# Kernel optimization log

Measured on AMD Instinct MI355X. Metric: run time of the kernel, lower is better.

The kernel has to match this reference:

```python
import jax, jax.numpy as jnp
import numpy as np

NUM_CLASSES = 80
CONF_THRE = 0.2
NMS_THRE = 0.45
MAX_DET = 300   # fixed cap replacing torch's variable-length NMS output (padded + keep mask)
IMG = 640.0


def setup_inputs() -> dict:
    key = jax.random.key(0)
    k1, k2 = jax.random.split(key)
    pred = jax.random.uniform(k1, (32, 8400, 85), dtype=jnp.float32)
    # scale cx,cy,w,h to pixel range so IoU/NMS geometry is realistic
    pred = pred.at[..., :4].multiply(IMG)
    zone = jax.random.uniform(k2, (8, 2), dtype=jnp.float32) * IMG
    return {"prediction": pred, "zone": zone}


def _pairwise_iou(b):
    # b: [B, K, 4] in x1y1x2y2
    area = jnp.clip(b[..., 2] - b[..., 0], 0.0) * jnp.clip(b[..., 3] - b[..., 1], 0.0)
    lt = jnp.maximum(b[:, :, None, :2], b[:, None, :, :2])
    rb = jnp.minimum(b[:, :, None, 2:], b[:, None, :, 2:])
    wh = jnp.clip(rb - lt, 0.0)
    inter = wh[..., 0] * wh[..., 1]
    return inter / (area[:, :, None] + area[:, None, :] - inter + 1e-9)


def _postprocess(prediction):
    # decode cx,cy,w,h -> x1,y1,x2,y2
    xy = prediction[..., :2]
    wh = prediction[..., 2:4]
    boxes = jnp.concatenate([xy - wh * 0.5, xy + wh * 0.5], axis=-1)  # [B,N,4]
    obj = prediction[..., 4]                                           # [B,N]
    cls = prediction[..., 5:5 + NUM_CLASSES]
    class_conf = jnp.max(cls, axis=-1)                                 # [B,N]
    class_pred = jnp.argmax(cls, axis=-1)                              # [B,N]

    # confidence mask (obj * class_conf >= thre); invalid -> -inf so top_k drops them
    nms_score = obj * class_conf
    nms_score = jnp.where(nms_score >= CONF_THRE, nms_score, -jnp.inf)

    s, idx = jax.lax.top_k(nms_score, MAX_DET)                         # [B,K]
    b = jnp.take_along_axis(boxes, idx[..., None], axis=1)             # [B,K,4]

    # class-agnostic greedy NMS on score-sorted boxes (matches torchvision.ops.nms)
    iou = _pairwise_iou(b)                                             # [B,K,K]
    keep = jnp.isfinite(s)                                             # valid (passed conf) entries
    ar = jnp.arange(MAX_DET)
    def body(i, keep):
        sup = keep[:, i][:, None] & (iou[:, i, :] > NMS_THRE) & (ar > i)
        return keep & jnp.logical_not(sup)
    keep = jax.lax.fori_loop(0, MAX_DET, body, keep)

    obj_s = jnp.take_along_axis(obj, idx, axis=1)
    conf_s = jnp.take_along_axis(class_conf, idx, axis=1)
    cls_s = jnp.take_along_axis(class_pred, idx, axis=1).astype(jnp.int32)
    # extract_boxes_scores_and_classes: score = max over columns [obj, class_conf]
    scores = jnp.maximum(obj_s, conf_s)
    return b, scores, cls_s, keep


def _points_inside_zone(px, py, zone):
    # px, py: [B,K]; zone: [Z,2]. Ray-casting parity test (faithful to torch version).
    zr = jnp.roll(zone, shift=1, axis=0)
    xi, yi = zone[:, 0], zone[:, 1]
    xj, yj = zr[:, 0], zr[:, 1]
    pyb = py[..., None]  # [B,K,1] vs [Z]
    pxb = px[..., None]
    gyi = yi > pyb
    gyj = yj > pyb
    gx = (xj - xi) * (pyb - yi) / (yj - yi) + xi
    inter = (gyi != gyj) & (gx > pxb)
    return (jnp.sum(inter.astype(jnp.int32), axis=-1) % 2) > 0


def reference(prediction, zone):
    b, scores, classes, keep = _postprocess(prediction)
    cx = (b[..., 0] + b[..., 2]) * 0.5
    cy = (b[..., 1] + b[..., 3]) * 0.5
    in_zone = _points_inside_zone(cx, cy, zone) & keep
    centers_yx = jnp.stack([cy, cx], axis=-1)                          # [B,K,2]
    boxes_yxyx = jnp.stack([b[..., 1], b[..., 0], b[..., 3], b[..., 2]], axis=-1)
    return boxes_yxyx, in_zone, scores, classes, centers_yx, keep
```

## Files before the change

kernel.cpp:

```cpp
#include <hip/hip_runtime.h>
#include <stdint.h>

typedef unsigned long long ull;

#define NA 8400
#define NB 32
#define KTOP 300
#define NC 80
#define CH 9
#define NCOPY 16
#define HSTRIDE 257

#define O1 38400
#define O2 48000
#define O3 57600
#define O4 67200
#define O5 86400

__global__ __launch_bounds__(256) void score_kernel(const float* __restrict__ pred,
                                                    uint32_t* __restrict__ keys) {
    __shared__ float sP[128 * 85];
    const int blk = blockIdx.x;
    const float4* g4 = (const float4*)(pred + (size_t)blk * 128 * 85);
    float4* l4 = (float4*)sP;
    for (int i = threadIdx.x; i < (128 * 85 / 4); i += 256) l4[i] = g4[i];
    __syncthreads();
    const int t = threadIdx.x;
    if (t < 128) {
        const float* p = sP + t * 85;
        float obj = p[4];
        float b0 = p[5], b1 = p[6], b2 = p[7], b3 = p[8];
        #pragma unroll
        for (int c = 4; c < NC; c += 4) {
            b0 = fmaxf(b0, p[5 + c]);
            b1 = fmaxf(b1, p[6 + c]);
            b2 = fmaxf(b2, p[7 + c]);
            b3 = fmaxf(b3, p[8 + c]);
        }
        float best = fmaxf(fmaxf(b0, b1), fmaxf(b2, b3));
        float sc = obj * best;
        uint32_t u = (sc >= 0.2f) ? (__float_as_uint(sc) | 0x80000000u) : 0x007FFFFFu;
        keys[(size_t)blk * 128 + t] = u;
    }
}

__global__ __launch_bounds__(1024) void batch_kernel(const float* __restrict__ pred,
                                                     const float* __restrict__ zone,
                                                     const uint32_t* __restrict__ keys,
                                                     float* __restrict__ out) {
    #pragma clang fp contract(off)
    __shared__ union {
        uint32_t keys[8448];
        struct {
            float b0[KTOP], b1[KTOP], b2[KTOP], b3[KTOP];
            ull mask[KTOP * 5];
        } late;
    } u;
    __shared__ ull sSel[KTOP];
    __shared__ ull sSorted[KTOP];
    __shared__ uint32_t sH[NCOPY * HSTRIDE];
    __shared__ uint32_t sWTot[16];
    __shared__ uint32_t sTot4[4];
    __shared__ uint32_t sBc[2];
    __shared__ int sCnt;
    __shared__ ull sKeepF[5];
    __shared__ float sZone[16];

    const int b = blockIdx.x;
    const int t = threadIdx.x;
    const int lane = t & 63;
    const int wv = t >> 6;

    {
        const uint4* g4 = (const uint4*)(keys + (size_t)b * NA);
        uint4* l4 = (uint4*)u.keys;
        for (int i = t; i < NA / 4; i += 1024) l4[i] = g4[i];
    }
    if (t < 16) sZone[t] = zone[t];
    if (t == 0) sCnt = 0;
    __syncthreads();

    uint32_t prefix = 0, r = KTOP;
    const int beg = t * CH;
    const int end = (beg + CH < NA) ? beg + CH : NA;
    for (int round = 0; round < 4; ++round) {
        const int shift = 24 - 8 * round;
        for (int i = t; i < NCOPY * HSTRIDE; i += 1024) sH[i] = 0u;
        __syncthreads();
        const uint32_t pmask = (round == 0) ? 0u : (0xFFFFFFFFu << (shift + 8));
        for (int e = beg; e < end; ++e) {
            uint32_t k = u.keys[e];
            if ((k & pmask) == (prefix & pmask))
                atomicAdd(&sH[wv * HSTRIDE + ((k >> shift) & 0xFFu)], 1u);
        }
        __syncthreads();
        uint32_t v = 0, s = 0;
        if (t < 256) {
            #pragma unroll
            for (int c = 0; c < NCOPY; ++c) v += sH[c * HSTRIDE + t];
            s = v;
            #pragma unroll
            for (int off = 1; off < 64; off <<= 1) {
                uint32_t o = __shfl_down(s, off, 64);
                if (lane + off < 64) s += o;
            }
            if (lane == 0) sTot4[t >> 6] = s;
        }
        __syncthreads();
        if (t < 256) {
            uint32_t S = s;
            const int w4 = t >> 6;
            #pragma unroll
            for (int w2 = 0; w2 < 4; ++w2) if (w2 > w4) S += sTot4[w2];
            uint32_t above = S - v;
            if (above < r && S >= r) {
                sBc[0] = prefix | ((uint32_t)t << shift);
                sBc[1] = r - above;
            }
        }
        __syncthreads();
        prefix = sBc[0]; r = sBc[1];
    }
    const uint32_t kth = prefix;
    const uint32_t rem = r;
    const uint32_t cntgt = KTOP - rem;

    {
        uint32_t eqc = 0;
        for (int e = beg; e < end; ++e) {
            uint32_t k = u.keys[e];
            if (k > kth) {
                int p = atomicAdd(&sCnt, 1);
                sSel[p] = ((ull)k << 32) | (ull)(0xFFFFFFFFu - (uint32_t)e);
            } else if (k == kth) eqc++;
        }
        uint32_t ps = eqc;
        #pragma unroll
        for (int off = 1; off < 64; off <<= 1) {
            uint32_t o = __shfl_up(ps, off, 64);
            if (lane >= off) ps += o;
        }
        if (lane == 63) sWTot[wv] = ps;
        __syncthreads();
        uint32_t off0 = ps - eqc;
        #pragma unroll
        for (int w2 = 0; w2 < 16; ++w2) if (w2 < wv) off0 += sWTot[w2];
        for (int e = beg; e < end; ++e) {
            uint32_t k = u.keys[e];
            if (k == kth) {
                if (off0 < rem)
                    sSel[cntgt + off0] = ((ull)k << 32) | (ull)(0xFFFFFFFFu - (uint32_t)e);
                off0++;
            }
        }
        __syncthreads();
    }

    if (t < KTOP) {
        ull my = sSel[t];
        int rk = 0;
        for (int j = 0; j < KTOP; ++j) {
            ull v = sSel[j];
            rk += (v > my) ? 1 : 0;
        }
        sSorted[rk] = my;
    }
    __syncthreads();

    const size_t bo = (size_t)b * KTOP;
    if (t < KTOP) {
        uint32_t a = 0xFFFFFFFFu - (uint32_t)sSorted[t];
        const float* p = pred + ((size_t)b * NA + a) * 85;
        float x = p[0], y = p[1], w = p[2], h = p[3], obj = p[4];
        float best = p[5]; int bc = 0;
        for (int c = 1; c < NC; ++c) {
            float v = p[5 + c];
            if (v > best) { best = v; bc = c; }
        }
        float hw = w * 0.5f, hh = h * 0.5f;
        float x1 = x - hw, y1 = y - hh, x2 = x + hw, y2 = y + hh;
        u.late.b0[t] = x1; u.late.b1[t] = y1;
        u.late.b2[t] = x2; u.late.b3[t] = y2;
        out[(bo + t) * 4 + 0] = y1;
        out[(bo + t) * 4 + 1] = x1;
        out[(bo + t) * 4 + 2] = y2;
        out[(bo + t) * 4 + 3] = x2;
        out[O4 + (bo + t) * 2 + 0] = (y1 + y2) * 0.5f;
        out[O4 + (bo + t) * 2 + 1] = (x1 + x2) * 0.5f;
        out[O2 + bo + t] = fmaxf(obj, best);
        out[O3 + bo + t] = (float)bc;
    }
    __syncthreads();

    for (int p = t; p < KTOP * 5; p += 1024) {
        const int i = p / 5;
        const int role = p % 5;
        const int j0 = role * 64;
        int jmax = j0 + 64; if (jmax > KTOP) jmax = KTOP;
        float x1 = u.late.b0[i], y1 = u.late.b1[i], x2 = u.late.b2[i], y2 = u.late.b3[i];
        float ai = fmaxf(x2 - x1, 0.0f) * fmaxf(y2 - y1, 0.0f);
        ull bits = 0ull;
        int jbeg = (j0 > i + 1) ? j0 : (i + 1);
        for (int j = jbeg; j < jmax; ++j) {
            float bx1 = u.late.b0[j], by1 = u.late.b1[j], bx2 = u.late.b2[j], by2 = u.late.b3[j];
            float aj = fmaxf(bx2 - bx1, 0.0f) * fmaxf(by2 - by1, 0.0f);
            float iw = fminf(x2, bx2) - fmaxf(x1, bx1); iw = fmaxf(iw, 0.0f);
            float ih = fminf(y2, by2) - fmaxf(y1, by1); ih = fmaxf(ih, 0.0f);
            float inter = iw * ih;
            float den = ai + aj;
            den = den - inter;
            den = den + 1e-9f;
            float iou = inter / den;
            if (iou > 0.45f) bits |= (1ull << (j - j0));
        }
        u.late.mask[p] = bits;
    }
    __syncthreads();

    if (wv == 0) {
        ull rm[5][5];
        ull kw[5];
        #pragma unroll
        for (int w = 0; w < 5; ++w) {
            int i = w * 64 + lane;
            bool f = (i < KTOP) && (((uint32_t)(sSorted[i] >> 32)) > 0x007FFFFFu);
            kw[w] = __ballot(f);
            #pragma unroll
            for (int ww = 0; ww < 5; ++ww)
                rm[w][ww] = (i < KTOP) ? u.late.mask[i * 5 + ww] : 0ull;
        }
        #pragma unroll
        for (int w = 0; w < 5; ++w) {
            ull cur = kw[w];
            while (cur) {
                int ib = __builtin_ctzll(cur);
                ull m0 = __shfl(rm[w][0], ib);
                ull m1 = __shfl(rm[w][1], ib);
                ull m2 = __shfl(rm[w][2], ib);
                ull m3 = __shfl(rm[w][3], ib);
                ull m4 = __shfl(rm[w][4], ib);
                kw[0] &= ~m0; kw[1] &= ~m1; kw[2] &= ~m2; kw[3] &= ~m3; kw[4] &= ~m4;
                ull done = (ib == 63) ? 0ull : (~0ull << (ib + 1));
                cur = kw[w] & done;
            }
        }
        if (lane == 0) {
            #pragma unroll
            for (int w = 0; w < 5; ++w) sKeepF[w] = kw[w];
        }
    }
    __syncthreads();

    if (t < KTOP) {
        int kp = (int)((sKeepF[t >> 6] >> (t & 63)) & 1ull);
        float cy = (u.late.b1[t] + u.late.b3[t]) * 0.5f;
        float cx = (u.late.b0[t] + u.late.b2[t]) * 0.5f;
        int cnt = 0;
        #pragma unroll
        for (int e = 0; e < 8; ++e) {
            float xi = sZone[2 * e], yi = sZone[2 * e + 1];
            int ep = (e + 7) & 7;
            float xj = sZone[2 * ep], yj = sZone[2 * ep + 1];
            bool gyi = yi > cy, gyj = yj > cy;
            if (gyi != gyj) {
                float gx = (xj - xi) * (cy - yi) / (yj - yi) + xi;
                if (gx > cx) cnt++;
            }
        }
        int inz = (((cnt & 1) != 0) && kp) ? 1 : 0;
        out[O1 + bo + t] = (float)inz;
        out[O5 + bo + t] = (float)kp;
    }
}

extern "C" void kernel_launch(void* const* d_in, const int* in_sizes, int n_in,
                              void* d_out, int out_size, void* d_ws, size_t ws_size,
                              hipStream_t stream) {
    const float* pred = (const float*)d_in[0];
    const float* zone = (const float*)d_in[1];
    float* out = (float*)d_out;
    uint32_t* keys = (uint32_t*)d_ws;

    score_kernel<<<(NB * NA) / 128, 256, 0, stream>>>(pred, keys);
    batch_kernel<<<NB, 1024, 0, stream>>>(pred, zone, keys, out);
}
```

Measured before the change: 200.3 us.

## Keep keys in registers and parallelize selection, ranking, argmax and zone test

Each thread now holds its 9 keys in registers instead of staging all keys in shared memory. The radix histogram scan runs in a single wave with one fewer barrier. Above-threshold selection uses a packed prefix scan instead of a shared atomic counter. Rank sorting is split across four threads per element, the class argmax is split between two lanes, and the zone test overlaps with the serial NMS wave. This adds register pressure, and the IoU loop now runs over full rows with a predicate instead of starting after the diagonal.

```diff
diff --git a/kernel.cpp b/kernel.cpp
--- a/kernel.cpp
+++ b/kernel.cpp
@@ -49,20 +49,15 @@
                                                      const uint32_t* __restrict__ keys,
                                                      float* __restrict__ out) {
     #pragma clang fp contract(off)
-    __shared__ union {
-        uint32_t keys[8448];
-        struct {
-            float b0[KTOP], b1[KTOP], b2[KTOP], b3[KTOP];
-            ull mask[KTOP * 5];
-        } late;
-    } u;
+    __shared__ float sB0[KTOP], sB1[KTOP], sB2[KTOP], sB3[KTOP];
+    __shared__ ull sMask[KTOP * 5];
     __shared__ ull sSel[KTOP];
     __shared__ ull sSorted[KTOP];
     __shared__ uint32_t sH[NCOPY * HSTRIDE];
     __shared__ uint32_t sWTot[16];
-    __shared__ uint32_t sTot4[4];
     __shared__ uint32_t sBc[2];
-    __shared__ int sCnt;
+    __shared__ uint32_t sRank[KTOP];
+    __shared__ uint32_t sPar[KTOP];
     __shared__ ull sKeepF[5];
     __shared__ float sZone[16];
 
@@ -71,52 +66,54 @@
     const int lane = t & 63;
     const int wv = t >> 6;
 
-    {
-        const uint4* g4 = (const uint4*)(keys + (size_t)b * NA);
-        uint4* l4 = (uint4*)u.keys;
-        for (int i = t; i < NA / 4; i += 1024) l4[i] = g4[i];
+    uint32_t myk[CH];
+    const int beg = t * CH;
+    #pragma unroll
+    for (int e = 0; e < CH; ++e) {
+        int idx = beg + e;
+        myk[e] = (idx < NA) ? keys[(size_t)b * NA + idx] : 0u;
     }
     if (t < 16) sZone[t] = zone[t];
-    if (t == 0) sCnt = 0;
-    __syncthreads();
+    if (t < KTOP) sRank[t] = 0u;
 
     uint32_t prefix = 0, r = KTOP;
-    const int beg = t * CH;
-    const int end = (beg + CH < NA) ? beg + CH : NA;
     for (int round = 0; round < 4; ++round) {
         const int shift = 24 - 8 * round;
         for (int i = t; i < NCOPY * HSTRIDE; i += 1024) sH[i] = 0u;
         __syncthreads();
         const uint32_t pmask = (round == 0) ? 0u : (0xFFFFFFFFu << (shift + 8));
-        for (int e = beg; e < end; ++e) {
-            uint32_t k = u.keys[e];
-            if ((k & pmask) == (prefix & pmask))
+        const uint32_t pref = prefix & pmask;
+        #pragma unroll
+        for (int e = 0; e < CH; ++e) {
+            uint32_t k = myk[e];
+            if ((k & pmask) == pref)
                 atomicAdd(&sH[wv * HSTRIDE + ((k >> shift) & 0xFFu)], 1u);
         }
         __syncthreads();
-        uint32_t v = 0, s = 0;
-        if (t < 256) {
+        if (wv == 0) {
+            uint32_t v0 = 0, v1 = 0, v2 = 0, v3 = 0;
             #pragma unroll
-            for (int c = 0; c < NCOPY; ++c) v += sH[c * HSTRIDE + t];
-            s = v;
+            for (int c = 0; c < NCOPY; ++c) {
+                const uint32_t* hc = &sH[c * HSTRIDE];
+                v0 += hc[lane]; v1 += hc[64 + lane];
+                v2 += hc[128 + lane]; v3 += hc[192 + lane];
+            }
+            uint32_t s0 = v0, s1 = v1, s2 = v2, s3 = v3;
             #pragma unroll
             for (int off = 1; off < 64; off <<= 1) {
-                uint32_t o = __shfl_down(s, off, 64);
-                if (lane + off < 64) s += o;
-            }
-            if (lane == 0) sTot4[t >> 6] = s;
-        }
-        __syncthreads();
-        if (t < 256) {
-            uint32_t S = s;
-            const int w4 = t >> 6;
-            #pragma unroll
-            for (int w2 = 0; w2 < 4; ++w2) if (w2 > w4) S += sTot4[w2];
-            uint32_t above = S - v;
-            if (above < r && S >= r) {
-                sBc[0] = prefix | ((uint32_t)t << shift);
-                sBc[1] = r - above;
-            }
+                uint32_t o0 = __shfl_down(s0, off, 64), o1 = __shfl_down(s1, off, 64);
+                uint32_t o2 = __shfl_down(s2, off, 64), o3 = __shfl_down(s3, off, 64);
+                if (lane + off < 64) { s0 += o0; s1 += o1; s2 += o2; s3 += o3; }
+            }
+            uint32_t T1 = __shfl(s1, 0, 64), T2 = __shfl(s2, 0, 64), T3 = __shfl(s3, 0, 64);
+            uint32_t S0 = s0 + T1 + T2 + T3;
+            uint32_t S1 = s1 + T2 + T3;
+            uint32_t S2 = s2 + T3;
+            uint32_t S3 = s3;
+            if (S0 >= r && S0 - v0 < r) { sBc[0] = prefix | ((uint32_t)lane << shift);         sBc[1] = r - (S0 - v0); }
+            if (S1 >= r && S1 - v1 < r) { sBc[0] = prefix | ((uint32_t)(64  + lane) << shift); sBc[1] = r - (S1 - v1); }
+            if (S2 >= r && S2 - v2 < r) { sBc[0] = prefix | ((uint32_t)(128 + lane) << shift); sBc[1] = r - (S2 - v2); }
+            if (S3 >= r && S3 - v3 < r) { sBc[0] = prefix | ((uint32_t)(192 + lane) << shift); sBc[1] = r - (S3 - v3); }
         }
         __syncthreads();
         prefix = sBc[0]; r = sBc[1];
@@ -126,15 +123,15 @@
     const uint32_t cntgt = KTOP - rem;
 
     {
-        uint32_t eqc = 0;
-        for (int e = beg; e < end; ++e) {
-            uint32_t k = u.keys[e];
-            if (k > kth) {
-                int p = atomicAdd(&sCnt, 1);
-                sSel[p] = ((ull)k << 32) | (ull)(0xFFFFFFFFu - (uint32_t)e);
-            } else if (k == kth) eqc++;
-        }
-        uint32_t ps = eqc;
+        uint32_t gtc = 0, eqc = 0;
+        #pragma unroll
+        for (int e = 0; e < CH; ++e) {
+            uint32_t k = myk[e];
+            gtc += (k > kth) ? 1u : 0u;
+            eqc += (k == kth) ? 1u : 0u;
+        }
+        uint32_t pack = (gtc << 16) | eqc;
+        uint32_t ps = pack;
         #pragma unroll
         for (int off = 1; off < 64; off <<= 1) {
             uint32_t o = __shfl_up(ps, off, 64);
@@ -142,67 +139,92 @@
         }
         if (lane == 63) sWTot[wv] = ps;
         __syncthreads();
-        uint32_t off0 = ps - eqc;
-        #pragma unroll
-        for (int w2 = 0; w2 < 16; ++w2) if (w2 < wv) off0 += sWTot[w2];
-        for (int e = beg; e < end; ++e) {
-            uint32_t k = u.keys[e];
-            if (k == kth) {
-                if (off0 < rem)
-                    sSel[cntgt + off0] = ((ull)k << 32) | (ull)(0xFFFFFFFFu - (uint32_t)e);
-                off0++;
-            }
-        }
-        __syncthreads();
-    }
-
-    if (t < KTOP) {
-        ull my = sSel[t];
-        int rk = 0;
-        for (int j = 0; j < KTOP; ++j) {
-            ull v = sSel[j];
-            rk += (v > my) ? 1 : 0;
-        }
-        sSorted[rk] = my;
-    }
+        uint32_t excl = ps - pack;
+        #pragma unroll
+        for (int w2 = 0; w2 < 16; ++w2) if (w2 < wv) excl += sWTot[w2];
+        uint32_t gtoff = excl >> 16;
+        uint32_t eqoff = excl & 0xFFFFu;
+        #pragma unroll
+        for (int e = 0; e < CH; ++e) {
+            uint32_t k = myk[e];
+            uint32_t idx = (uint32_t)(beg + e);
+            if (k > kth) {
+                sSel[gtoff++] = ((ull)k << 32) | (ull)(0xFFFFFFFFu - idx);
+            } else if (k == kth) {
+                if (eqoff < rem)
+                    sSel[cntgt + eqoff] = ((ull)k << 32) | (ull)(0xFFFFFFFFu - idx);
+                eqoff++;
+            }
+        }
+        __syncthreads();
+    }
+
+    for (int p2 = t; p2 < KTOP * 4; p2 += 1024) {
+        const int i = p2 >> 2;
+        const int q = p2 & 3;
+        const ull my = sSel[i];
+        const int j0 = q * 75, j1 = j0 + 75;
+        uint32_t cnt = 0;
+        for (int j = j0; j < j1; ++j)
+            cnt += (sSel[j] > my) ? 1u : 0u;
+        if (cnt) atomicAdd(&sRank[i], cnt);
+    }
+    __syncthreads();
+    if (t < KTOP) sSorted[sRank[t]] = sSel[t];
     __syncthreads();
 
     const size_t bo = (size_t)b * KTOP;
-    if (t < KTOP) {
-        uint32_t a = 0xFFFFFFFFu - (uint32_t)sSorted[t];
+    if (t < 2 * KTOP) {
+        const int row = t >> 1;
+        const int half = t & 1;
+        const uint32_t a = 0xFFFFFFFFu - (uint32_t)sSorted[row];
         const float* p = pred + ((size_t)b * NA + a) * 85;
-        float x = p[0], y = p[1], w = p[2], h = p[3], obj = p[4];
-        float best = p[5]; int bc = 0;
-        for (int c = 1; c < NC; ++c) {
-            float v = p[5 + c];
-            if (v > best) { best = v; bc = c; }
-        }
-        float hw = w * 0.5f, hh = h * 0.5f;
-        float x1 = x - hw, y1 = y - hh, x2 = x + hw, y2 = y + hh;
-        u.late.b0[t] = x1; u.late.b1[t] = y1;
-        u.late.b2[t] = x2; u.late.b3[t] = y2;
-        out[(bo + t) * 4 + 0] = y1;
-        out[(bo + t) * 4 + 1] = x1;
-        out[(bo + t) * 4 + 2] = y2;
-        out[(bo + t) * 4 + 3] = x2;
-        out[O4 + (bo + t) * 2 + 0] = (y1 + y2) * 0.5f;
-        out[O4 + (bo + t) * 2 + 1] = (x1 + x2) * 0.5f;
-        out[O2 + bo + t] = fmaxf(obj, best);
-        out[O3 + bo + t] = (float)bc;
-    }
-    __syncthreads();
-
-    for (int p = t; p < KTOP * 5; p += 1024) {
-        const int i = p / 5;
-        const int role = p % 5;
+        const int cbase = half * 40;
+        float v0 = p[5 + cbase], v1 = p[6 + cbase], v2 = p[7 + cbase], v3 = p[8 + cbase];
+        int   c0 = cbase, c1 = cbase + 1, c2 = cbase + 2, c3 = cbase + 3;
+        #pragma unroll
+        for (int c = 4; c < 40; c += 4) {
+            float w0 = p[5 + cbase + c],     w1 = p[6 + cbase + c];
+            float w2 = p[7 + cbase + c],     w3 = p[8 + cbase + c];
+            if (w0 > v0) { v0 = w0; c0 = cbase + c; }
+            if (w1 > v1) { v1 = w1; c1 = cbase + c + 1; }
+            if (w2 > v2) { v2 = w2; c2 = cbase + c + 2; }
+            if (w3 > v3) { v3 = w3; c3 = cbase + c + 3; }
+        }
+        float bv = v0; int bc = c0;
+        if (v1 > bv || (v1 == bv && c1 < bc)) { bv = v1; bc = c1; }
+        if (v2 > bv || (v2 == bv && c2 < bc)) { bv = v2; bc = c2; }
+        if (v3 > bv || (v3 == bv && c3 < bc)) { bv = v3; bc = c3; }
+        float pv = __shfl_xor(bv, 1, 64);
+        int   pc = __shfl_xor(bc, 1, 64);
+        if (half == 0) {
+            if (pv > bv) { bv = pv; bc = pc; }
+            float x = p[0], y = p[1], w = p[2], h = p[3], obj = p[4];
+            float hw = w * 0.5f, hh = h * 0.5f;
+            float x1 = x - hw, y1 = y - hh, x2 = x + hw, y2 = y + hh;
+            sB0[row] = x1; sB1[row] = y1; sB2[row] = x2; sB3[row] = y2;
+            out[(bo + row) * 4 + 0] = y1;
+            out[(bo + row) * 4 + 1] = x1;
+            out[(bo + row) * 4 + 2] = y2;
+            out[(bo + row) * 4 + 3] = x2;
+            out[O4 + (bo + row) * 2 + 0] = (y1 + y2) * 0.5f;
+            out[O4 + (bo + row) * 2 + 1] = (x1 + x2) * 0.5f;
+            out[O2 + bo + row] = fmaxf(obj, bv);
+            out[O3 + bo + row] = (float)bc;
+        }
+    }
+    __syncthreads();
+
+    for (int p2 = t; p2 < KTOP * 5; p2 += 1024) {
+        const int role = p2 / KTOP;
+        const int i = p2 - role * KTOP;
         const int j0 = role * 64;
         int jmax = j0 + 64; if (jmax > KTOP) jmax = KTOP;
-        float x1 = u.late.b0[i], y1 = u.late.b1[i], x2 = u.late.b2[i], y2 = u.late.b3[i];
+        float x1 = sB0[i], y1 = sB1[i], x2 = sB2[i], y2 = sB3[i];
         float ai = fmaxf(x2 - x1, 0.0f) * fmaxf(y2 - y1, 0.0f);
         ull bits = 0ull;
-        int jbeg = (j0 > i + 1) ? j0 : (i + 1);
-        for (int j = jbeg; j < jmax; ++j) {
-            float bx1 = u.late.b0[j], by1 = u.late.b1[j], bx2 = u.late.b2[j], by2 = u.late.b3[j];
+        for (int j = j0; j < jmax; ++j) {
+            float bx1 = sB0[j], by1 = sB1[j], bx2 = sB2[j], by2 = sB3[j];
             float aj = fmaxf(bx2 - bx1, 0.0f) * fmaxf(by2 - by1, 0.0f);
             float iw = fminf(x2, bx2) - fmaxf(x1, bx1); iw = fmaxf(iw, 0.0f);
             float ih = fminf(y2, by2) - fmaxf(y1, by1); ih = fmaxf(ih, 0.0f);
@@ -211,9 +233,9 @@
             den = den - inter;
             den = den + 1e-9f;
             float iou = inter / den;
-            if (iou > 0.45f) bits |= (1ull << (j - j0));
-        }
-        u.late.mask[p] = bits;
+            if (j > i && iou > 0.45f) bits |= (1ull << (j - j0));
+        }
+        sMask[i * 5 + role] = bits;
     }
     __syncthreads();
 
@@ -227,7 +249,7 @@
             kw[w] = __ballot(f);
             #pragma unroll
             for (int ww = 0; ww < 5; ++ww)
-                rm[w][ww] = (i < KTOP) ? u.late.mask[i * 5 + ww] : 0ull;
+                rm[w][ww] = (i < KTOP) ? sMask[i * 5 + ww] : 0ull;
         }
         #pragma unroll
         for (int w = 0; w < 5; ++w) {
@@ -248,13 +270,10 @@
             #pragma unroll
             for (int w = 0; w < 5; ++w) sKeepF[w] = kw[w];
         }
-    }
-    __syncthreads();
-
-    if (t < KTOP) {
-        int kp = (int)((sKeepF[t >> 6] >> (t & 63)) & 1ull);
-        float cy = (u.late.b1[t] + u.late.b3[t]) * 0.5f;
-        float cx = (u.late.b0[t] + u.late.b2[t]) * 0.5f;
+    } else if (t >= 512 && t < 512 + KTOP) {
+        const int i = t - 512;
+        float cy = (sB1[i] + sB3[i]) * 0.5f;
+        float cx = (sB0[i] + sB2[i]) * 0.5f;
         int cnt = 0;
         #pragma unroll
         for (int e = 0; e < 8; ++e) {
@@ -267,7 +286,13 @@
                 if (gx > cx) cnt++;
             }
         }
-        int inz = (((cnt & 1) != 0) && kp) ? 1 : 0;
+        sPar[i] = (uint32_t)(cnt & 1);
+    }
+    __syncthreads();
+
+    if (t < KTOP) {
+        int kp = (int)((sKeepF[t >> 6] >> (t & 63)) & 1ull);
+        int inz = (sPar[t] && kp) ? 1 : 0;
         out[O1 + bo + t] = (float)inz;
         out[O5 + bo + t] = (float)kp;
     }
```

Measured after the change: 205.3 us. 2.5% more time.
